# Kernel tuning notes

Measured on AMD Instinct MI355X. Metric: run time of the kernel, lower is better.

## Reference

```python
import jax, jax.numpy as jnp
import numpy as np

IN_FEATURES = 8192
OUT_FEATURES = 4096
NNZ = 4194304
N_COLS = 4096  # must equal OUT_FEATURES so torch's bias broadcast is valid


def setup_inputs() -> dict:
    key = jax.random.key(0)
    k1, k2, k3, k4, k5 = jax.random.split(key, 5)
    values = jax.random.normal(k1, (NNZ,), dtype=jnp.float32)
    bias = jax.random.normal(k2, (OUT_FEATURES,), dtype=jnp.float32)
    x = jax.random.normal(k3, (OUT_FEATURES, N_COLS), dtype=jnp.float32)
    rows = jax.random.randint(k4, (NNZ,), 0, IN_FEATURES, dtype=jnp.int32)
    cols = jax.random.randint(k5, (NNZ,), 0, OUT_FEATURES, dtype=jnp.int32)
    return {"values": values, "bias": bias, "x": x, "rows": rows, "cols": cols}


def reference(values, bias, x, rows, cols):
    # Densify the COO sparse weight; duplicate coordinates are summed,
    # matching torch.sparse COO semantics.
    W = jnp.zeros((IN_FEATURES, OUT_FEATURES), dtype=x.dtype).at[rows, cols].add(values)
    # torch.sparse.addmm(bias, W, x) = bias + W @ x
    # result: [IN_FEATURES, N_COLS]; bias [OUT_FEATURES] broadcasts over the
    # last axis (valid because N_COLS == OUT_FEATURES, as in the original).
    return bias + W @ x
```

## Files before the change

kernel.cpp:

```cpp
#include <hip/hip_runtime.h>

#define M_DIM 8192
#define K_DIM 4096
#define N_DIM 4096
#define NNZ_CNT 4194304
#define GRID_X 16
#define GRID_Y 32

#define BINS 2048
#define BIN_ROWS 4
#define NBLK 512
#define CHUNK 8192
#define RSV 24

typedef __attribute__((ext_vector_type(8))) short bf16x8;
typedef __attribute__((ext_vector_type(4))) float f32x4;

__device__ __forceinline__ unsigned short f2bf(float f) {
  unsigned int u = __float_as_uint(f);
  unsigned int r = (u + 0x7FFFu + ((u >> 16) & 1u)) >> 16;
  return (unsigned short)r;
}

__device__ __forceinline__ void gload_lds16(const void* g, void* l) {
  __builtin_amdgcn_global_load_lds(
      (const __attribute__((address_space(1))) void*)g,
      (__attribute__((address_space(3))) void*)l, 16, 0, 0);
}

__global__ __launch_bounds__(256) void bin_scatter(
    const float* __restrict__ vals,
    const int* __restrict__ rows,
    const int* __restrict__ cols,
    unsigned int* __restrict__ packets,
    unsigned int* __restrict__ counts) {
  __shared__ unsigned int lcur[BINS];
  const int blk = blockIdx.x;
  const int tid = threadIdx.x;
#pragma unroll 8
  for (int b = tid; b < BINS; b += 256) lcur[b] = 0;
  __syncthreads();
  const int base = blk * CHUNK;
  const int4* r4 = (const int4*)(rows + base);
  const int4* c4 = (const int4*)(cols + base);
  const float4* v4 = (const float4*)(vals + base);
  unsigned int* wnd = packets + (long)blk * BINS * RSV;
#pragma unroll 2
  for (int it = 0; it < CHUNK / 4 / 256; ++it) {
    int idx = it * 256 + tid;
    int4 r = r4[idx];
    int4 c = c4[idx];
    float4 v = v4[idx];
#pragma unroll
    for (int e = 0; e < 4; ++e) {
      int rr = (&r.x)[e], cc = (&c.x)[e];
      float vv = (&v.x)[e];
      unsigned int pk = (unsigned int)f2bf(vv) |
                        ((unsigned int)cc << 16) |
                        ((unsigned int)(rr & (BIN_ROWS - 1)) << 28);
      int bin = rr >> 2;
      unsigned int slot = atomicAdd(&lcur[bin], 1u);
      if (slot < RSV) wnd[(unsigned)bin * RSV + slot] = pk;
    }
  }
  __syncthreads();
#pragma unroll 8
  for (int b = tid; b < BINS; b += 256)
    counts[blk * BINS + b] = lcur[b];
}

__global__ __launch_bounds__(256) void apply_bins(
    const unsigned int* __restrict__ packets,
    const unsigned int* __restrict__ counts,
    unsigned int* __restrict__ Wb2) {
  extern __shared__ float acc[];
  const int bin = blockIdx.x;
  const int tid = threadIdx.x;
  float4* a4 = (float4*)acc;
#pragma unroll 4
  for (int i = tid; i < BIN_ROWS * K_DIM / 4; i += 256)
    a4[i] = float4{0.f, 0.f, 0.f, 0.f};
  __syncthreads();
#pragma unroll
  for (int half = 0; half < 2; ++half) {
    const int blk = tid + half * 256;
    unsigned int cnt = counts[blk * BINS + bin];
    if (cnt > RSV) cnt = RSV;
    const unsigned int* seg = packets + ((long)blk * BINS + bin) * RSV;
    for (unsigned int i = 0; i < cnt; ++i) {
      unsigned int pk = seg[i];
      float v = __uint_as_float(pk << 16);
      int c = (pk >> 16) & 0xFFF;
      int r2 = pk >> 28;
      atomicAdd(&acc[r2 * K_DIM + c], v);
    }
  }
  __syncthreads();
  unsigned int* dst = Wb2 + (long)bin * (BIN_ROWS * K_DIM / 2);
#pragma unroll 4
  for (int i = tid; i < BIN_ROWS * K_DIM / 2; i += 256) {
    float lo = acc[2 * i], hi = acc[2 * i + 1];
    dst[i] = (unsigned int)f2bf(lo) | ((unsigned int)f2bf(hi) << 16);
  }
}

__global__ __launch_bounds__(256) void transpose_cvt(
    const float* __restrict__ x, unsigned short* __restrict__ xT) {
  __shared__ float tile[64][65];
  const int nb = blockIdx.x * 64;
  const int kb = blockIdx.y * 64;
  const int tx = threadIdx.x & 15;
  const int ty = threadIdx.x >> 4;
#pragma unroll
  for (int i = 0; i < 4; ++i) {
    const int k = ty + 16 * i;
    float4 v = *(const float4*)&x[(long)(kb + k) * N_DIM + nb + 4 * tx];
    tile[k][4 * tx + 0] = v.x; tile[k][4 * tx + 1] = v.y;
    tile[k][4 * tx + 2] = v.z; tile[k][4 * tx + 3] = v.w;
  }
  __syncthreads();
#pragma unroll
  for (int i = 0; i < 4; ++i) {
    const int n = ty + 16 * i;
    ushort4 o;
    o.x = f2bf(tile[4 * tx + 0][n]);
    o.y = f2bf(tile[4 * tx + 1][n]);
    o.z = f2bf(tile[4 * tx + 2][n]);
    o.w = f2bf(tile[4 * tx + 3][n]);
    *(ushort4*)&xT[(long)(nb + n) * K_DIM + kb + 4 * tx] = o;
  }
}


#define LDS_BUF   65536
#define LDS_B_OFF 32768

template<bool STA, bool STB, bool FIN>
__device__ __forceinline__ void tile_body(
    int u, int cur,
    const unsigned short* __restrict__ Ag, const unsigned short* __restrict__ Bg,
    char* smem, int st16,
    int a_off0, int a_off1, int b_off0, int b_off1,
    bf16x8 (&a)[4][2], bf16x8 (&b)[4][2], f32x4 (&acc)[8][4]) {
  char* Acur = smem + cur * LDS_BUF;
  char* Bcur = Acur + LDS_B_OFF;
  char* Aoth = smem + (cur ^ 1) * LDS_BUF;
  const unsigned short* Asrc = Ag + (long)(u + 1) * 64;
  const unsigned short* Bsrc = Bg + (long)(u + 2) * 64;

#pragma unroll
  for (int m = 0; m < 4; ++m) {
    a[m][0] = *(const bf16x8*)(Acur + m * 2048 + a_off0);
    a[m][1] = *(const bf16x8*)(Acur + m * 2048 + a_off1);
  }
#pragma unroll
  for (int n = 0; n < 2; ++n) {
    b[n][0] = *(const bf16x8*)(Bcur + n * 2048 + b_off0);
    b[n][1] = *(const bf16x8*)(Bcur + n * 2048 + b_off1);
  }
  if (STA) {
    gload_lds16(Asrc, Aoth + st16);
    gload_lds16(Asrc + (long)64 * K_DIM, Aoth + 8192 + st16);
  }
  __builtin_amdgcn_s_barrier();
  asm volatile("s_waitcnt lgkmcnt(0)" ::: "memory");
  __builtin_amdgcn_sched_barrier(0);
  __builtin_amdgcn_s_setprio(1);
#pragma unroll
  for (int m = 0; m < 4; ++m)
#pragma unroll
    for (int n = 0; n < 2; ++n) {
      acc[m][n] = __builtin_amdgcn_mfma_f32_16x16x32_bf16(a[m][0], b[n][0], acc[m][n], 0, 0, 0);
      acc[m][n] = __builtin_amdgcn_mfma_f32_16x16x32_bf16(a[m][1], b[n][1], acc[m][n], 0, 0, 0);
    }
  __builtin_amdgcn_s_setprio(0);
  __builtin_amdgcn_s_barrier();

#pragma unroll
  for (int n = 2; n < 4; ++n) {
    b[n][0] = *(const bf16x8*)(Bcur + n * 2048 + b_off0);
    b[n][1] = *(const bf16x8*)(Bcur + n * 2048 + b_off1);
  }
  if (STA) {
    gload_lds16(Asrc + (long)128 * K_DIM, Aoth + 16384 + st16);
    gload_lds16(Asrc + (long)192 * K_DIM, Aoth + 24576 + st16);
  }
  __builtin_amdgcn_s_barrier();
  asm volatile("s_waitcnt lgkmcnt(0)" ::: "memory");
  __builtin_amdgcn_sched_barrier(0);
  __builtin_amdgcn_s_setprio(1);
#pragma unroll
  for (int m = 0; m < 4; ++m)
#pragma unroll
    for (int n = 2; n < 4; ++n) {
      acc[m][n] = __builtin_amdgcn_mfma_f32_16x16x32_bf16(a[m][0], b[n][0], acc[m][n], 0, 0, 0);
      acc[m][n] = __builtin_amdgcn_mfma_f32_16x16x32_bf16(a[m][1], b[n][1], acc[m][n], 0, 0, 0);
    }
  __builtin_amdgcn_s_setprio(0);
  __builtin_amdgcn_s_barrier();

#pragma unroll
  for (int m = 0; m < 4; ++m) {
    a[m][0] = *(const bf16x8*)(Acur + (m + 4) * 2048 + a_off0);
    a[m][1] = *(const bf16x8*)(Acur + (m + 4) * 2048 + a_off1);
  }
  if (STB) {
    gload_lds16(Bsrc, Bcur + st16);
    gload_lds16(Bsrc + (long)64 * K_DIM, Bcur + 8192 + st16);
  }
  __builtin_amdgcn_s_barrier();
  asm volatile("s_waitcnt lgkmcnt(0)" ::: "memory");
  __builtin_amdgcn_sched_barrier(0);
  __builtin_amdgcn_s_setprio(1);
#pragma unroll
  for (int m = 0; m < 4; ++m)
#pragma unroll
    for (int n = 0; n < 2; ++n) {
      acc[m + 4][n] = __builtin_amdgcn_mfma_f32_16x16x32_bf16(a[m][0], b[n][0], acc[m + 4][n], 0, 0, 0);
      acc[m + 4][n] = __builtin_amdgcn_mfma_f32_16x16x32_bf16(a[m][1], b[n][1], acc[m + 4][n], 0, 0, 0);
    }
  __builtin_amdgcn_s_setprio(0);
  __builtin_amdgcn_s_barrier();

  if (STB) {
    gload_lds16(Bsrc + (long)128 * K_DIM, Bcur + 16384 + st16);
    gload_lds16(Bsrc + (long)192 * K_DIM, Bcur + 24576 + st16);
  }
  if (FIN) asm volatile("s_waitcnt vmcnt(0)" ::: "memory");
  else     asm volatile("s_waitcnt vmcnt(4)" ::: "memory");
  __builtin_amdgcn_s_barrier();
  __builtin_amdgcn_s_setprio(1);
#pragma unroll
  for (int m = 0; m < 4; ++m)
#pragma unroll
    for (int n = 2; n < 4; ++n) {
      acc[m + 4][n] = __builtin_amdgcn_mfma_f32_16x16x32_bf16(a[m][0], b[n][0], acc[m + 4][n], 0, 0, 0);
      acc[m + 4][n] = __builtin_amdgcn_mfma_f32_16x16x32_bf16(a[m][1], b[n][1], acc[m + 4][n], 0, 0, 0);
    }
  __builtin_amdgcn_s_setprio(0);
  __builtin_amdgcn_s_barrier();
}

__global__ __launch_bounds__(512, 2) void gemm8(
    const unsigned short* __restrict__ A,
    const unsigned short* __restrict__ B,
    const float* __restrict__ bias,
    float* __restrict__ C) {
  extern __shared__ __align__(16) char smem[];
  const int tid = threadIdx.x;
  const int lane = tid & 63;
  const int wid = tid >> 6;
  const int wr = wid >> 2, wc = wid & 3;

  const int wg0 = blockIdx.y * GRID_X + blockIdx.x;
  const int swz = (wg0 & 7) * (GRID_X * GRID_Y / 8) + (wg0 >> 3);
  const int bm0 = (swz >> 4) * 256;
  const int bn0 = (swz & 15) * 256;

  const int srow = tid >> 3;
  const int pcb = (tid & 7) << 4;
  const int scol = (pcb ^ ((srow & 7) << 4)) >> 1;
  const unsigned short* Ag = A + (long)(bm0 + srow) * K_DIM + scol;
  const unsigned short* Bg = B + (long)(bn0 + srow) * K_DIM + scol;
  const int st16 = tid * 16;

  const int q = (lane >> 4) << 4;
  const int s = (lane & 7) << 4;
  const int qs = q ^ s;
  const int a_off0 = (wr * 128 + (lane & 15)) * 128 + qs;
  const int a_off1 = a_off0 ^ 64;
  const int b_off0 = (wc * 64 + (lane & 15)) * 128 + qs;
  const int b_off1 = b_off0 ^ 64;

  f32x4 acc[8][4] = {};
  bf16x8 a[4][2], b[4][2];

#pragma unroll
  for (int h = 0; h < 2; ++h)
#pragma unroll
    for (int r = 0; r < 2; ++r) {
      gload_lds16(Ag + (long)(h * 128 + r * 64) * K_DIM,
                  smem + h * 16384 + r * 8192 + st16);
      gload_lds16(Bg + (long)(h * 128 + r * 64) * K_DIM,
                  smem + LDS_B_OFF + h * 16384 + r * 8192 + st16);
    }
#pragma unroll
  for (int h = 0; h < 2; ++h)
#pragma unroll
    for (int r = 0; r < 2; ++r)
      gload_lds16(Bg + (long)(h * 128 + r * 64) * K_DIM + 64,
                  smem + LDS_BUF + LDS_B_OFF + h * 16384 + r * 8192 + st16);
  asm volatile("s_waitcnt vmcnt(4)" ::: "memory");
  __builtin_amdgcn_s_barrier();

#pragma unroll 1
  for (int u2 = 0; u2 < 31; ++u2) {
    tile_body<true, true, false>(2 * u2, 0, Ag, Bg, smem, st16,
                                 a_off0, a_off1, b_off0, b_off1, a, b, acc);
    tile_body<true, true, false>(2 * u2 + 1, 1, Ag, Bg, smem, st16,
                                 a_off0, a_off1, b_off0, b_off1, a, b, acc);
  }
  tile_body<true, false, true>(62, 0, Ag, Bg, smem, st16,
                               a_off0, a_off1, b_off0, b_off1, a, b, acc);
  tile_body<false, false, true>(63, 1, Ag, Bg, smem, st16,
                                a_off0, a_off1, b_off0, b_off1, a, b, acc);

#pragma unroll
  for (int n = 0; n < 4; ++n) {
    const int col = bn0 + wc * 64 + n * 16 + (lane & 15);
    const float bv = bias[col];
#pragma unroll
    for (int m = 0; m < 8; ++m) {
      const int r0 = bm0 + wr * 128 + m * 16 + (lane >> 4) * 4;
#pragma unroll
      for (int j = 0; j < 4; ++j)
        __builtin_nontemporal_store(acc[m][n][j] + bv,
                                    &C[(long)(r0 + j) * N_DIM + col]);
    }
  }
}

extern "C" void kernel_launch(void* const* d_in, const int* in_sizes, int n_in,
                              void* d_out, int out_size, void* d_ws, size_t ws_size,
                              hipStream_t stream) {
  const float* values = (const float*)d_in[0];
  const float* bias   = (const float*)d_in[1];
  const float* x      = (const float*)d_in[2];
  const int*   rows   = (const int*)d_in[3];
  const int*   cols   = (const int*)d_in[4];
  float* out = (float*)d_out;

  unsigned short* Wb = (unsigned short*)d_ws;
  unsigned short* xT = (unsigned short*)((char*)d_ws + (size_t)M_DIM * K_DIM * 2);

  unsigned int* packets = (unsigned int*)d_out;
  unsigned int* counts = (unsigned int*)((char*)d_out + (112u << 20));

  hipFuncSetAttribute((const void*)gemm8,
                      hipFuncAttributeMaxDynamicSharedMemorySize, 131072);
  hipFuncSetAttribute((const void*)apply_bins,
                      hipFuncAttributeMaxDynamicSharedMemorySize, 65536);

  bin_scatter<<<NBLK, 256, 0, stream>>>(values, rows, cols, packets, counts);
  apply_bins<<<BINS, 256, 65536, stream>>>(packets, counts, (unsigned int*)Wb);
  transpose_cvt<<<dim3(N_DIM / 64, K_DIM / 64), 256, 0, stream>>>(x, xT);
  gemm8<<<dim3(GRID_X, GRID_Y), 512, 131072, stream>>>(Wb, xT, bias, out);
}
```

Before: 367.0 us.

## Fuse bin scatter with x transpose and vectorize bin apply loads/stores

Merges the COO binning kernel and the x transpose/bf16 conversion into one launch, dispatching on block index so both independent preprocessing stages run concurrently and one kernel launch is removed. Vectorizes packet reads in apply_bins as uint4 and writes the packed bf16 weight rows as 16-byte stores. Replaces the nontemporal output stores in the GEMM epilogue with ordinary stores. The fused kernel uses a shared buffer sized for the transpose tile (16.6KB vs 8KB for binning), which may lower occupancy for the scatter blocks.

```diff
diff --git a/kernel.cpp b/kernel.cpp
--- a/kernel.cpp
+++ b/kernel.cpp
@@ -12,6 +12,7 @@
 #define NBLK 512
 #define CHUNK 8192
 #define RSV 24
+#define TRANS_BLKS 4096
 
 typedef __attribute__((ext_vector_type(8))) short bf16x8;
 typedef __attribute__((ext_vector_type(4))) float f32x4;
@@ -22,51 +23,86 @@
   return (unsigned short)r;
 }
 
+__device__ __forceinline__ unsigned int pack2(float a, float b) {
+  return (unsigned int)f2bf(a) | ((unsigned int)f2bf(b) << 16);
+}
+
 __device__ __forceinline__ void gload_lds16(const void* g, void* l) {
   __builtin_amdgcn_global_load_lds(
       (const __attribute__((address_space(1))) void*)g,
       (__attribute__((address_space(3))) void*)l, 16, 0, 0);
 }
 
-__global__ __launch_bounds__(256) void bin_scatter(
+__global__ __launch_bounds__(256) void fused_pre(
     const float* __restrict__ vals,
     const int* __restrict__ rows,
     const int* __restrict__ cols,
     unsigned int* __restrict__ packets,
-    unsigned int* __restrict__ counts) {
-  __shared__ unsigned int lcur[BINS];
-  const int blk = blockIdx.x;
+    unsigned int* __restrict__ counts,
+    const float* __restrict__ x,
+    unsigned short* __restrict__ xT) {
+  __shared__ __align__(16) char smraw[64 * 65 * 4];
   const int tid = threadIdx.x;
+
+  if (blockIdx.x < NBLK) {
+    unsigned int* lcur = (unsigned int*)smraw;
+    const int blk = blockIdx.x;
 #pragma unroll 8
-  for (int b = tid; b < BINS; b += 256) lcur[b] = 0;
-  __syncthreads();
-  const int base = blk * CHUNK;
-  const int4* r4 = (const int4*)(rows + base);
-  const int4* c4 = (const int4*)(cols + base);
-  const float4* v4 = (const float4*)(vals + base);
-  unsigned int* wnd = packets + (long)blk * BINS * RSV;
+    for (int b = tid; b < BINS; b += 256) lcur[b] = 0;
+    __syncthreads();
+    const int base = blk * CHUNK;
+    const int4* r4 = (const int4*)(rows + base);
+    const int4* c4 = (const int4*)(cols + base);
+    const float4* v4 = (const float4*)(vals + base);
+    unsigned int* wnd = packets + (long)blk * BINS * RSV;
 #pragma unroll 2
-  for (int it = 0; it < CHUNK / 4 / 256; ++it) {
-    int idx = it * 256 + tid;
-    int4 r = r4[idx];
-    int4 c = c4[idx];
-    float4 v = v4[idx];
-#pragma unroll
-    for (int e = 0; e < 4; ++e) {
-      int rr = (&r.x)[e], cc = (&c.x)[e];
-      float vv = (&v.x)[e];
-      unsigned int pk = (unsigned int)f2bf(vv) |
-                        ((unsigned int)cc << 16) |
-                        ((unsigned int)(rr & (BIN_ROWS - 1)) << 28);
-      int bin = rr >> 2;
-      unsigned int slot = atomicAdd(&lcur[bin], 1u);
-      if (slot < RSV) wnd[(unsigned)bin * RSV + slot] = pk;
-    }
-  }
-  __syncthreads();
+    for (int it = 0; it < CHUNK / 4 / 256; ++it) {
+      int idx = it * 256 + tid;
+      int4 r = r4[idx];
+      int4 c = c4[idx];
+      float4 v = v4[idx];
+#pragma unroll
+      for (int e = 0; e < 4; ++e) {
+        int rr = (&r.x)[e], cc = (&c.x)[e];
+        float vv = (&v.x)[e];
+        unsigned int pk = (unsigned int)f2bf(vv) |
+                          ((unsigned int)cc << 16) |
+                          ((unsigned int)(rr & (BIN_ROWS - 1)) << 28);
+        int bin = rr >> 2;
+        unsigned int slot = atomicAdd(&lcur[bin], 1u);
+        if (slot < RSV) wnd[(unsigned)bin * RSV + slot] = pk;
+      }
+    }
+    __syncthreads();
 #pragma unroll 8
-  for (int b = tid; b < BINS; b += 256)
-    counts[blk * BINS + b] = lcur[b];
+    for (int b = tid; b < BINS; b += 256)
+      counts[blk * BINS + b] = lcur[b];
+  } else {
+    float (*tile)[65] = (float(*)[65])smraw;
+    const int t = blockIdx.x - NBLK;
+    const int nb = (t & 63) * 64;
+    const int kb = (t >> 6) * 64;
+    const int tx = tid & 15;
+    const int ty = tid >> 4;
+#pragma unroll
+    for (int i = 0; i < 4; ++i) {
+      const int k = ty + 16 * i;
+      float4 v = *(const float4*)&x[(long)(kb + k) * N_DIM + nb + 4 * tx];
+      tile[k][4 * tx + 0] = v.x; tile[k][4 * tx + 1] = v.y;
+      tile[k][4 * tx + 2] = v.z; tile[k][4 * tx + 3] = v.w;
+    }
+    __syncthreads();
+#pragma unroll
+    for (int i = 0; i < 4; ++i) {
+      const int n = ty + 16 * i;
+      ushort4 o;
+      o.x = f2bf(tile[4 * tx + 0][n]);
+      o.y = f2bf(tile[4 * tx + 1][n]);
+      o.z = f2bf(tile[4 * tx + 2][n]);
+      o.w = f2bf(tile[4 * tx + 3][n]);
+      *(ushort4*)&xT[(long)(nb + n) * K_DIM + kb + 4 * tx] = o;
+    }
+  }
 }
 
 __global__ __launch_bounds__(256) void apply_bins(
@@ -86,48 +122,31 @@
     const int blk = tid + half * 256;
     unsigned int cnt = counts[blk * BINS + bin];
     if (cnt > RSV) cnt = RSV;
-    const unsigned int* seg = packets + ((long)blk * BINS + bin) * RSV;
-    for (unsigned int i = 0; i < cnt; ++i) {
-      unsigned int pk = seg[i];
-      float v = __uint_as_float(pk << 16);
-      int c = (pk >> 16) & 0xFFF;
-      int r2 = pk >> 28;
-      atomicAdd(&acc[r2 * K_DIM + c], v);
+    const uint4* seg4 = (const uint4*)(packets + ((long)blk * BINS + bin) * RSV);
+    for (unsigned int v = 0; v * 4 < cnt; ++v) {
+      uint4 pkv = seg4[v];
+#pragma unroll
+      for (int e = 0; e < 4; ++e) {
+        unsigned int i = v * 4 + e;
+        if (i < cnt) {
+          unsigned int pk = (&pkv.x)[e];
+          float val = __uint_as_float(pk << 16);
+          int c = (pk >> 16) & 0xFFF;
+          int r2 = pk >> 28;
+          atomicAdd(&acc[r2 * K_DIM + c], val);
+        }
+      }
     }
   }
   __syncthreads();
-  unsigned int* dst = Wb2 + (long)bin * (BIN_ROWS * K_DIM / 2);
+  uint4* dst4 = (uint4*)(Wb2 + (long)bin * (BIN_ROWS * K_DIM / 2));
 #pragma unroll 4
-  for (int i = tid; i < BIN_ROWS * K_DIM / 2; i += 256) {
-    float lo = acc[2 * i], hi = acc[2 * i + 1];
-    dst[i] = (unsigned int)f2bf(lo) | ((unsigned int)f2bf(hi) << 16);
-  }
-}
-
-__global__ __launch_bounds__(256) void transpose_cvt(
-    const float* __restrict__ x, unsigned short* __restrict__ xT) {
-  __shared__ float tile[64][65];
-  const int nb = blockIdx.x * 64;
-  const int kb = blockIdx.y * 64;
-  const int tx = threadIdx.x & 15;
-  const int ty = threadIdx.x >> 4;
-#pragma unroll
-  for (int i = 0; i < 4; ++i) {
-    const int k = ty + 16 * i;
-    float4 v = *(const float4*)&x[(long)(kb + k) * N_DIM + nb + 4 * tx];
-    tile[k][4 * tx + 0] = v.x; tile[k][4 * tx + 1] = v.y;
-    tile[k][4 * tx + 2] = v.z; tile[k][4 * tx + 3] = v.w;
-  }
-  __syncthreads();
-#pragma unroll
-  for (int i = 0; i < 4; ++i) {
-    const int n = ty + 16 * i;
-    ushort4 o;
-    o.x = f2bf(tile[4 * tx + 0][n]);
-    o.y = f2bf(tile[4 * tx + 1][n]);
-    o.z = f2bf(tile[4 * tx + 2][n]);
-    o.w = f2bf(tile[4 * tx + 3][n]);
-    *(ushort4*)&xT[(long)(nb + n) * K_DIM + kb + 4 * tx] = o;
+  for (int i = tid; i < BIN_ROWS * K_DIM / 8; i += 256) {
+    float4 lo = a4[2 * i], hi = a4[2 * i + 1];
+    uint4 o;
+    o.x = pack2(lo.x, lo.y); o.y = pack2(lo.z, lo.w);
+    o.z = pack2(hi.x, hi.y); o.w = pack2(hi.z, hi.w);
+    dst4[i] = o;
   }
 }
 
@@ -314,8 +333,7 @@
       const int r0 = bm0 + wr * 128 + m * 16 + (lane >> 4) * 4;
 #pragma unroll
       for (int j = 0; j < 4; ++j)
-        __builtin_nontemporal_store(acc[m][n][j] + bv,
-                                    &C[(long)(r0 + j) * N_DIM + col]);
+        C[(long)(r0 + j) * N_DIM + col] = acc[m][n][j] + bv;
     }
   }
 }
@@ -341,8 +359,8 @@
   hipFuncSetAttribute((const void*)apply_bins,
                       hipFuncAttributeMaxDynamicSharedMemorySize, 65536);
 
-  bin_scatter<<<NBLK, 256, 0, stream>>>(values, rows, cols, packets, counts);
+  fused_pre<<<NBLK + TRANS_BLKS, 256, 0, stream>>>(values, rows, cols,
+                                                   packets, counts, x, xT);
   apply_bins<<<BINS, 256, 65536, stream>>>(packets, counts, (unsigned int*)Wb);
-  transpose_cvt<<<dim3(N_DIM / 64, K_DIM / 64), 256, 0, stream>>>(x, xT);
   gemm8<<<dim3(GRID_X, GRID_Y), 512, 131072, stream>>>(Wb, xT, bias, out);
 }
```

Result: faster. 337.3 us, median of 2 (-8.1%).
